# Optimization experiments

Measured on AMD Instinct MI355X. Metric: run time of the kernel, lower is better.

Reference implementation:

```python
import jax, jax.numpy as jnp
import numpy as np

NQ, NT, BSZ, E, NH = 100, 197, 128, 768, 12
HD = E // NH
EPS = 1e-12  # torch F.normalize default eps


def _l2norm(x, axis=-1):
    n = jnp.linalg.norm(x, axis=axis, keepdims=True)
    return x / jnp.maximum(n, EPS)


def setup_inputs() -> dict:
    rng = jax.random.key(0)
    ks = jax.random.split(rng, 10)
    s = 0.02  # xavier-ish scale for weights
    return {
        "query": jax.random.normal(ks[0], (NQ, BSZ, E), jnp.float32),
        "key": jax.random.normal(ks[1], (NT, BSZ, E), jnp.float32),
        "value": jax.random.normal(ks[2], (NT, BSZ, E), jnp.float32),
        "in_proj_weight": jax.random.normal(ks[3], (3 * E, E), jnp.float32) * s,
        "in_proj_bias": jnp.zeros((3 * E,), jnp.float32),
        "out_proj_weight": jax.random.normal(ks[4], (E, E), jnp.float32) * s,
        "out_proj_bias": jnp.zeros((E,), jnp.float32),
        "temperature": jnp.ones((NH, 1, 1), jnp.float32),
        "q_mapper": jax.random.normal(ks[5], (1, NT, NQ), jnp.float32),
        "x_mapper": jax.random.normal(ks[6], (1, NQ, NT), jnp.float32),
    }


def reference(query, key, value, in_proj_weight, in_proj_bias,
              out_proj_weight, out_proj_bias, temperature, q_mapper, x_mapper):
    nq, bsz, e = query.shape
    nt = key.shape[0]
    # packed in-projection: split into q/k/v weights
    wq, wk, wv = jnp.split(in_proj_weight, 3, axis=0)
    bq, bk, bv = jnp.split(in_proj_bias, 3, axis=0)
    q = query @ wq.T + bq   # [Nq, bsz, E]
    k = key @ wk.T + bk     # [Nt, bsz, E]
    v = value @ wv.T + bv   # [Nt, bsz, E]
    # reshape to [bsz, nh, hd, N] (channel-major for cross-covariance attn)
    q = q.reshape(nq, bsz, NH, HD).transpose(1, 2, 3, 0)  # [b, h, d, Nq]
    k = k.reshape(nt, bsz, NH, HD).transpose(1, 2, 3, 0)  # [b, h, d, Nt]
    v = v.reshape(nt, bsz, NH, HD).transpose(1, 2, 3, 0)  # [b, h, d, Nt]
    # normalize channel vectors over tokens
    qn = _l2norm(q)
    kn = _l2norm(k)
    # mappers: normalize over last dim, then shape to [Nq, Nt] operators
    qm_op = _l2norm(q_mapper[0])  # [Nt, Nq] normalized over Nq; transpose below
    xm_op = _l2norm(x_mapper[0])  # [Nq, Nt] normalized over Nt
    # qm = q @ q_mapper^T : [b,h,d,Nq] x [Nq,Nt] -> [b,h,d,Nt]
    qm = jnp.einsum('bhdq,tq->bhdt', qn, qm_op)
    # cross-covariance attention over channels: [b,h,d,d]
    attn = jnp.einsum('bhdt,bhet->bhde', qm, kn) * temperature[None]  # temp [nh,1,1] broadcasts per-head
    attn = jax.nn.softmax(attn, axis=-1)
    x = jnp.einsum('bhde,bhet->bhdt', attn, v)        # [b,h,d,Nt]
    out = jnp.einsum('bhdt,qt->bhdq', x, xm_op)       # [b,h,d,Nq]
    # back to [Nq, bsz, E]
    out = out.transpose(3, 0, 1, 2).reshape(nq, bsz, e)
    out = out @ out_proj_weight.T + out_proj_bias
    return out
```

## Files before the change

kernel.cpp:

```cpp
#include <hip/hip_runtime.h>
#include <hip/hip_bf16.h>

using bf16 = __hip_bfloat16;

constexpr int NQ  = 100;
constexpr int NT  = 197;
constexpr int BSZ = 128;
constexpr int EMB = 768;
constexpr int NHD = 12;
constexpr int HDD = 64;
constexpr int COLS = BSZ * EMB;
constexpr int M_Q  = NQ * BSZ;
constexpr int M_KV = NT * BSZ;
constexpr int TPAD = 224;

constexpr size_t SZ_Q16  = (size_t)M_Q  * EMB * 2;
constexpr size_t SZ_KV16 = (size_t)M_KV * EMB * 2;
constexpr size_t SZ_WI   = (size_t)3 * EMB * EMB * 2;
constexpr size_t SZ_T16  = (size_t)COLS * TPAD * 2;
constexpr size_t SZ_128  = (size_t)COLS * 128 * 2;
constexpr size_t OFF_QB   = 256;
constexpr size_t OFF_KB   = OFF_QB + SZ_Q16;
constexpr size_t OFF_VB   = OFF_KB + SZ_KV16;
constexpr size_t OFF_WI   = OFF_VB + SZ_KV16;
constexpr size_t OFF_QP16 = OFF_WI + SZ_WI;
constexpr size_t OFF_KP16 = OFF_QP16 + SZ_Q16;
constexpr size_t OFF_VP16 = OFF_KP16 + SZ_KV16;
constexpr size_t OFF_QMNT = OFF_VP16 + SZ_KV16;
constexpr size_t OFF_XMNT = OFF_QMNT + 57344;
constexpr size_t OFF_WO   = OFF_XMNT + 57344;
constexpr size_t OFF_KPT  = 256;
constexpr size_t OFF_VPT  = OFF_KPT + SZ_T16;
constexpr size_t OFF_W16T = OFF_VPT + SZ_T16;
constexpr size_t OFF_QNT  = OFF_KP16;
constexpr size_t OFF_G16  = OFF_VP16;
constexpr size_t OFF_XO   = 256;

__device__ __forceinline__ float dl(const float* p) { return *p; }
__device__ __forceinline__ float dl(const bf16* p) { return __bfloat162float(*p); }

__device__ __forceinline__ ushort f2bf(float x) {
    union { float f; unsigned u; } v; v.f = x;
    unsigned r = v.u + 0x7FFFu + ((v.u >> 16) & 1u);
    return (ushort)(r >> 16);
}
__device__ __forceinline__ float bf2f(ushort x) {
    union { unsigned u; float f; } v; v.u = (unsigned)x << 16;
    return v.f;
}
__device__ __forceinline__ void dstore(float* p, float v) { *p = v; }
__device__ __forceinline__ void dstore(bf16* p, float v) { *p = __float2bfloat16(v); }

typedef __attribute__((ext_vector_type(8))) short short8;
typedef __attribute__((ext_vector_type(4))) short shortv4;
typedef __attribute__((ext_vector_type(4))) float f32x4;

__device__ __forceinline__ void gload16(const bf16* g, ushort* l) {
    __builtin_amdgcn_global_load_lds(
        (const __attribute__((address_space(1))) unsigned int*)g,
        (__attribute__((address_space(3))) unsigned int*)l, 16, 0, 0);
}

__device__ __forceinline__ int2 xcd_swz(int bx, int by, int gx, int gy) {
    const int nwg = gx * gy;
    const int L = by * gx + bx;
    const int q = nwg >> 3, r = nwg & 7;
    const int c = L & 7, i = L >> 3;
    const int wg = (c < r ? c * (q + 1) : r * (q + 1) + (c - r) * q) + i;
    return make_int2(wg % gx, wg / gx);
}

__global__ void k_zero(float* p, int n) {
    int i = blockIdx.x * 256 + threadIdx.x;
    if (i < n) p[i] = 0.f;
}

__global__ __launch_bounds__(256) void k_cvt5(
        const float* __restrict__ s0, bf16* __restrict__ d0,
        const float* __restrict__ s1, bf16* __restrict__ d1,
        const float* __restrict__ s2, bf16* __restrict__ d2,
        const float* __restrict__ s3, bf16* __restrict__ d3,
        const float* __restrict__ s4, bf16* __restrict__ d4) {
    int bk = blockIdx.x;
    const float* s; bf16* d; int lb;
    if      (bk < 864)   { s = s0; d = d0; lb = bk; }
    else if (bk < 5664)  { s = s1; d = d1; lb = bk - 864; }
    else if (bk < 15120) { s = s2; d = d2; lb = bk - 5664; }
    else if (bk < 24576) { s = s3; d = d3; lb = bk - 15120; }
    else                 { s = s4; d = d4; lb = bk - 24576; }
    size_t i = ((size_t)lb * 256 + threadIdx.x) * 8;
    float4 a = *(const float4*)(s + i), b = *(const float4*)(s + i + 4);
    short8 r;
    r[0] = (short)f2bf(a.x); r[1] = (short)f2bf(a.y); r[2] = (short)f2bf(a.z); r[3] = (short)f2bf(a.w);
    r[4] = (short)f2bf(b.x); r[5] = (short)f2bf(b.y); r[6] = (short)f2bf(b.z); r[7] = (short)f2bf(b.w);
    *(short8*)(d + i) = r;
}

template <typename T>
__global__ __launch_bounds__(128) void k_qmn(const T* qm, bf16* dstT) {
    __shared__ float red[128];
    int t = blockIdx.x, q = threadIdx.x;
    float v = (q < NQ) ? dl(&qm[t * NQ + q]) : 0.f;
    red[q] = v * v;
    __syncthreads();
    for (int s = 64; s > 0; s >>= 1) { if (q < s) red[q] += red[q + s]; __syncthreads(); }
    float inv = 1.f / fmaxf(sqrtf(red[0]), 1e-12f);
    if (q < NQ) dstore(&dstT[(size_t)q * TPAD + t], v * inv);
}

template <typename T>
__global__ __launch_bounds__(256) void k_xmn(const T* xm, bf16* dstT) {
    __shared__ float red[256];
    int q = blockIdx.x, t = threadIdx.x;
    float v = (t < NT) ? dl(&xm[q * NT + t]) : 0.f;
    red[t] = v * v;
    __syncthreads();
    for (int s = 128; s > 0; s >>= 1) { if (t < s) red[t] += red[t + s]; __syncthreads(); }
    float inv = 1.f / fmaxf(sqrtf(red[0]), 1e-12f);
    if (t < NT) dstore(&dstT[(size_t)q * TPAD + t], v * inv);
}

template <int NR, int TP, int NORM>
__global__ __launch_bounds__(256) void k_trn(const bf16* __restrict__ src,
        bf16* __restrict__ dst) {
    __shared__ ushort tile[TP * 73];
    __shared__ float ssp[4][64];
    __shared__ float inv_s[64];
    const int col0 = blockIdx.x * 64;
    const int tid = threadIdx.x;
    const int c = tid & 63, tb = tid >> 6;
    float ss = 0.f;
#pragma unroll
    for (int it = 0; it < TP / 4; ++it) {
        int t = tb + it * 4;
        ushort v = 0;
        if (t < NR) v = *(const ushort*)&src[(size_t)t * COLS + col0 + c];
        tile[t * 73 + c] = v;
        if (NORM) { float f = bf2f(v); ss = fmaf(f, f, ss); }
    }
    if (NORM) {
        ssp[tb][c] = ss;
        __syncthreads();
        if (tid < 64) {
            float s = ssp[0][tid] + ssp[1][tid] + ssp[2][tid] + ssp[3][tid];
            inv_s[tid] = 1.f / fmaxf(sqrtf(s), 1e-12f);
        }
    }
    __syncthreads();
    constexpr int UPC = TP / 8;
#pragma unroll
    for (int it = 0; it < (64 * UPC) / 256; ++it) {
        int u = tid + it * 256;
        int cc = u / UPC, t0 = (u % UPC) * 8;
        float inv = NORM ? inv_s[cc] : 1.f;
        short8 s;
#pragma unroll
        for (int r = 0; r < 8; ++r) {
            ushort raw = tile[(t0 + r) * 73 + cc];
            s[r] = NORM ? (short)f2bf(bf2f(raw) * inv) : (short)raw;
        }
        *(short8*)&dst[(size_t)(col0 + cc) * TP + t0] = s;
    }
}

__global__ __launch_bounds__(256) void k_trn2(const bf16* __restrict__ kp,
        const bf16* __restrict__ vp, bf16* __restrict__ kpT, bf16* __restrict__ vpT) {
    __shared__ ushort tile[TPAD * 73];
    __shared__ float ssp[4][64];
    __shared__ float inv_s[64];
    const int bk = blockIdx.x;
    const bool vseg = bk >= 1536;
    const bf16* src = vseg ? vp : kp;
    bf16* dst = vseg ? vpT : kpT;
    const int col0 = (vseg ? bk - 1536 : bk) * 64;
    const int tid = threadIdx.x;
    const int c = tid & 63, tb = tid >> 6;
    float ss = 0.f;
#pragma unroll
    for (int it = 0; it < TPAD / 4; ++it) {
        int t = tb + it * 4;
        ushort v = 0;
        if (t < NT) v = *(const ushort*)&src[(size_t)t * COLS + col0 + c];
        tile[t * 73 + c] = v;
        if (!vseg) { float f = bf2f(v); ss = fmaf(f, f, ss); }
    }
    if (!vseg) {
        ssp[tb][c] = ss;
        __syncthreads();
        if (tid < 64) {
            float s = ssp[0][tid] + ssp[1][tid] + ssp[2][tid] + ssp[3][tid];
            inv_s[tid] = 1.f / fmaxf(sqrtf(s), 1e-12f);
        }
    }
    __syncthreads();
    constexpr int UPC = TPAD / 8;
#pragma unroll
    for (int it = 0; it < (64 * UPC) / 256; ++it) {
        int u = tid + it * 256;
        int cc = u / UPC, t0 = (u % UPC) * 8;
        float inv = vseg ? 1.f : inv_s[cc];
        short8 s;
#pragma unroll
        for (int r = 0; r < 8; ++r) {
            ushort raw = tile[(t0 + r) * 73 + cc];
            s[r] = vseg ? (short)raw : (short)f2bf(bf2f(raw) * inv);
        }
        *(short8*)&dst[(size_t)(col0 + cc) * TPAD + t0] = s;
    }
}

template <typename TBias>
__global__ __launch_bounds__(256) void k_proj(
        const bf16* __restrict__ Aq, const bf16* __restrict__ Ak, const bf16* __restrict__ Av,
        const bf16* __restrict__ Wi, bf16* __restrict__ Cq, bf16* __restrict__ Ck,
        bf16* __restrict__ Cv, const TBias* __restrict__ bias) {
    __shared__ __align__(16) ushort As[128 * 32];
    __shared__ __align__(16) ushort Bs[128 * 32];
    const int t = threadIdx.x;
    const int2 bxy = xcd_swz(blockIdx.x, blockIdx.y, gridDim.x, gridDim.y);
    int byy = bxy.y, seg, lby;
    if (byy < 100)      { seg = 0; lby = byy; }
    else if (byy < 297) { seg = 1; lby = byy - 100; }
    else                { seg = 2; lby = byy - 297; }
    const bf16* Ab = seg == 0 ? Aq : (seg == 1 ? Ak : Av);
    const bf16* Wb = Wi + (size_t)seg * EMB * EMB;
    bf16* C = seg == 0 ? Cq : (seg == 1 ? Ck : Cv);
    const TBias* bp = bias + seg * EMB;
    const int n0 = bxy.x * 128, m0 = lby * 128;
    const int ln = t & 63, wv = t >> 6;
    const int ln15 = ln & 15, q8 = ln >> 4;
    const int mw = (wv & 1) * 64, nw = (wv >> 1) * 64;

    const int sr = ln >> 2, sk = (ln & 3) * 8;
    const bf16* gA = Ab + (size_t)(m0 + wv * 32 + sr) * EMB + sk;
    const bf16* gB = Wb + (size_t)(n0 + wv * 32 + sr) * EMB + sk;
    const size_t r16 = (size_t)16 * EMB;
    ushort* lA = &As[wv * 1024];
    ushort* lB = &Bs[wv * 1024];

    f32x4 acc[4][4] = {};
    for (int k0 = 0; k0 < EMB; k0 += 32) {
        gload16(gA + k0,       lA);
        gload16(gA + r16 + k0, lA + 512);
        gload16(gB + k0,       lB);
        gload16(gB + r16 + k0, lB + 512);
        __syncthreads();
        short8 a[4], b[4];
#pragma unroll
        for (int i = 0; i < 4; ++i)
            a[i] = *(const short8*)&As[(mw + i * 16 + ln15) * 32 + q8 * 8];
#pragma unroll
        for (int j = 0; j < 4; ++j)
            b[j] = *(const short8*)&Bs[(nw + j * 16 + ln15) * 32 + q8 * 8];
#pragma unroll
        for (int i = 0; i < 4; ++i)
#pragma unroll
            for (int j = 0; j < 4; ++j)
                acc[i][j] = __builtin_amdgcn_mfma_f32_16x16x32_bf16(a[i], b[j], acc[i][j], 0, 0, 0);
        __syncthreads();
    }
#pragma unroll
    for (int j = 0; j < 4; ++j) {
        const int n = n0 + nw + j * 16 + ln15;
        const float bv = dl(&bp[n]);
#pragma unroll
        for (int i = 0; i < 4; ++i) {
            const int mb = m0 + mw + i * 16 + q8 * 4;
#pragma unroll
            for (int r = 0; r < 4; ++r)
                dstore(&C[(size_t)(mb + r) * EMB + n], acc[i][j][r] + bv);
        }
    }
}

__global__ __launch_bounds__(256) void k_gw(
        const bf16* __restrict__ kpT, const bf16* __restrict__ vpT,
        const bf16* __restrict__ qmnT, const bf16* __restrict__ xmnT,
        bf16* __restrict__ g16, bf16* __restrict__ w16T) {
    __shared__ __align__(16) ushort As[128 * 32];
    __shared__ __align__(16) ushort Bs[128 * 32];
    const int t = threadIdx.x;
    const int2 bxy = xcd_swz(blockIdx.x, blockIdx.y, gridDim.x, gridDim.y);
    const bool wseg = bxy.y >= 768;
    const int lby = wseg ? bxy.y - 768 : bxy.y;
    const bf16* Ab = wseg ? vpT : kpT;
    const bf16* Bb = wseg ? xmnT : qmnT;
    const int m0 = lby * 128;
    const int ln = t & 63, wv = t >> 6;
    const int ln15 = ln & 15, q8 = ln >> 4;
    const int mw = (wv & 1) * 64, nw = (wv >> 1) * 64;

    const int sr = ln >> 2, sk = (ln & 3) * 8;
    const bf16* gA = Ab + (size_t)(m0 + wv * 32 + sr) * TPAD + sk;
    const bf16* gB = Bb + (size_t)(wv * 32 + sr) * TPAD + sk;
    const size_t r16 = (size_t)16 * TPAD;
    ushort* lA = &As[wv * 1024];
    ushort* lB = &Bs[wv * 1024];

    f32x4 acc[4][4] = {};
    for (int k0 = 0; k0 < TPAD; k0 += 32) {
        gload16(gA + k0,       lA);
        gload16(gA + r16 + k0, lA + 512);
        gload16(gB + k0,       lB);
        gload16(gB + r16 + k0, lB + 512);
        __syncthreads();
        short8 a[4], b[4];
#pragma unroll
        for (int i = 0; i < 4; ++i)
            a[i] = *(const short8*)&As[(mw + i * 16 + ln15) * 32 + q8 * 8];
#pragma unroll
        for (int j = 0; j < 4; ++j)
            b[j] = *(const short8*)&Bs[(nw + j * 16 + ln15) * 32 + q8 * 8];
#pragma unroll
        for (int i = 0; i < 4; ++i)
#pragma unroll
            for (int j = 0; j < 4; ++j)
                acc[i][j] = __builtin_amdgcn_mfma_f32_16x16x32_bf16(a[i], b[j], acc[i][j], 0, 0, 0);
        __syncthreads();
    }
#pragma unroll
    for (int j = 0; j < 4; ++j) {
        const int n = nw + j * 16 + ln15;
#pragma unroll
        for (int i = 0; i < 4; ++i) {
            const int mb = m0 + mw + i * 16 + q8 * 4;
            if (wseg) {
                shortv4 s;
#pragma unroll
                for (int r = 0; r < 4; ++r) s[r] = (short)f2bf(acc[i][j][r]);
                *(shortv4*)&w16T[(size_t)n * COLS + mb] = s;
            } else {
#pragma unroll
                for (int r = 0; r < 4; ++r)
                    dstore(&g16[(size_t)(mb + r) * 128 + n], acc[i][j][r]);
            }
        }
    }
}

template <typename TC, typename TBias>
__global__ __launch_bounds__(256) void k_gemm_mfma(
        const bf16* __restrict__ Ab, const bf16* __restrict__ Wb,
        TC* __restrict__ C, const TBias* __restrict__ bias,
        int M, int N, int K, int ldc) {
    __shared__ __align__(16) ushort As[128 * 32];
    __shared__ __align__(16) ushort Bs[128 * 32];
    const int t = threadIdx.x;
    const int2 bxy = xcd_swz(blockIdx.x, blockIdx.y, gridDim.x, gridDim.y);
    const int n0 = bxy.x * 128, m0 = bxy.y * 128;
    const int ln = t & 63, wv = t >> 6;
    const int ln15 = ln & 15, q8 = ln >> 4;
    const int mw = (wv & 1) * 64, nw = (wv >> 1) * 64;

    const int sr = ln >> 2, sk = (ln & 3) * 8;
    const bf16* gA = Ab + (size_t)(m0 + wv * 32 + sr) * K + sk;
    const bf16* gB = Wb + (size_t)(n0 + wv * 32 + sr) * K + sk;
    const size_t r16 = (size_t)16 * K;
    ushort* lA = &As[wv * 1024];
    ushort* lB = &Bs[wv * 1024];

    f32x4 acc[4][4] = {};
    for (int k0 = 0; k0 < K; k0 += 32) {
        gload16(gA + k0,       lA);
        gload16(gA + r16 + k0, lA + 512);
        gload16(gB + k0,       lB);
        gload16(gB + r16 + k0, lB + 512);
        __syncthreads();
        short8 a[4], b[4];
#pragma unroll
        for (int i = 0; i < 4; ++i)
            a[i] = *(const short8*)&As[(mw + i * 16 + ln15) * 32 + q8 * 8];
#pragma unroll
        for (int j = 0; j < 4; ++j)
            b[j] = *(const short8*)&Bs[(nw + j * 16 + ln15) * 32 + q8 * 8];
#pragma unroll
        for (int i = 0; i < 4; ++i)
#pragma unroll
            for (int j = 0; j < 4; ++j)
                acc[i][j] = __builtin_amdgcn_mfma_f32_16x16x32_bf16(a[i], b[j], acc[i][j], 0, 0, 0);
        __syncthreads();
    }
#pragma unroll
    for (int j = 0; j < 4; ++j) {
        const int n = n0 + nw + j * 16 + ln15;
        const float bv = dl(&bias[n]);
#pragma unroll
        for (int i = 0; i < 4; ++i) {
            const int mb = m0 + mw + i * 16 + q8 * 4;
#pragma unroll
            for (int r = 0; r < 4; ++r)
                dstore(&C[(size_t)(mb + r) * ldc + n], acc[i][j][r] + bv);
        }
    }
}

template <typename T>
__global__ __launch_bounds__(256) void k_attn(
        const bf16* __restrict__ qnT, const bf16* __restrict__ g16,
        const bf16* __restrict__ w16T, const T* __restrict__ temp,
        bf16* __restrict__ xo) {
    const int h = blockIdx.x, b = blockIdx.y;
    const int tid = threadIdx.x;
    const int ln = tid & 63, wv = tid >> 6;
    const int ln15 = ln & 15, q8 = ln >> 4;
    const int colbase = b * EMB + h * HDD;
    __shared__ __align__(16) ushort smem[16384];
    char* sm = (char*)smem;

#pragma unroll
    for (int it = 0; it < 4; ++it) {
        int u = tid + it * 256;
        int e = u >> 4, q0 = (u & 15) * 8;
        short8 s = *(const short8*)&g16[(size_t)(colbase + e) * 128 + q0];
        *(short8*)(sm + ((e * 256 + q0 * 2) ^ ((e & 7) << 4))) = s;
    }
#pragma unroll
    for (int it = 0; it < 4; ++it) {
        int u = tid + it * 256;
        int d = u >> 4, q0 = (u & 15) * 8;
        short8 s = *(const short8*)&qnT[(size_t)(colbase + d) * 128 + q0];
        *(short8*)(sm + 16384 + ((d * 256 + q0 * 2) ^ ((d & 7) << 4))) = s;
    }
    __syncthreads();

    const int drow = 16 * wv + ln15;
    f32x4 acc[4] = {};
#pragma unroll
    for (int ks = 0; ks < 4; ++ks) {
        short8 bfrag = *(const short8*)(sm + 16384 +
            ((drow * 256 + ks * 64 + q8 * 16) ^ ((drow & 7) << 4)));
#pragma unroll
        for (int i = 0; i < 4; ++i) {
            int erow = i * 16 + ln15;
            short8 afrag = *(const short8*)(sm +
                ((erow * 256 + ks * 64 + q8 * 16) ^ ((erow & 7) << 4)));
            acc[i] = __builtin_amdgcn_mfma_f32_16x16x32_bf16(afrag, bfrag, acc[i], 0, 0, 0);
        }
    }

    const float tv = dl(&temp[h]);
    float p[4][4];
    float mx = -1e30f;
#pragma unroll
    for (int i = 0; i < 4; ++i)
#pragma unroll
        for (int r = 0; r < 4; ++r) { p[i][r] = acc[i][r] * tv; mx = fmaxf(mx, p[i][r]); }
    mx = fmaxf(mx, __shfl_xor(mx, 16, 64));
    mx = fmaxf(mx, __shfl_xor(mx, 32, 64));
    float sum = 0.f;
#pragma unroll
    for (int i = 0; i < 4; ++i)
#pragma unroll
        for (int r = 0; r < 4; ++r) { p[i][r] = __expf(p[i][r] - mx); sum += p[i][r]; }
    sum += __shfl_xor(sum, 16, 64);
    sum += __shfl_xor(sum, 32, 64);
    const float rs = 1.f / sum;

    __syncthreads();

#pragma unroll
    for (int i = 0; i < 4; ++i) {
        shortv4 s4;
#pragma unroll
        for (int r = 0; r < 4; ++r) s4[r] = (short)f2bf(p[i][r] * rs);
        *(shortv4*)(sm + 16384 + drow * 144 + q8 * 8 + 32 * i) = s4;
    }
#pragma unroll
    for (int it = 0; it < 4; ++it) {
        int u = tid + it * 256;
        int q = u >> 3, e0 = (u & 7) * 8;
        short8 s = *(const short8*)&w16T[(size_t)q * COLS + colbase + e0];
        *(short8*)(sm + ((q * 128 + e0 * 2) ^ ((q & 7) << 4))) = s;
    }
    __syncthreads();

    f32x4 o[7] = {};
#pragma unroll
    for (int ks = 0; ks < 2; ++ks) {
        short8 afrag = *(const short8*)(sm + 16384 + drow * 144 + ks * 64 + q8 * 16);
#pragma unroll
        for (int j = 0; j < 7; ++j) {
            int qrow = j * 16 + ln15;
            short8 bfrag = *(const short8*)(sm +
                ((qrow * 128 + ks * 64 + q8 * 16) ^ ((qrow & 7) << 4)));
            o[j] = __builtin_amdgcn_mfma_f32_16x16x32_bf16(afrag, bfrag, o[j], 0, 0, 0);
        }
    }
    const int dbase = h * HDD + 16 * wv + q8 * 4;
#pragma unroll
    for (int j = 0; j < 7; ++j) {
        int q = j * 16 + ln15;
        if (q < NQ) {
            shortv4 s4;
#pragma unroll
            for (int r = 0; r < 4; ++r) s4[r] = (short)f2bf(o[j][r]);
            *(shortv4*)&xo[(size_t)(q * BSZ + b) * EMB + dbase] = s4;
        }
    }
}

extern "C" void kernel_launch(void* const* d_in, const int* in_sizes, int n_in,
                              void* d_out, int out_size, void* d_ws, size_t ws_size,
                              hipStream_t stream) {
    char* ws = (char*)d_ws;
    bf16* qb16  = (bf16*)(ws + OFF_QB);
    bf16* kb16  = (bf16*)(ws + OFF_KB);
    bf16* vb16  = (bf16*)(ws + OFF_VB);
    bf16* wi16  = (bf16*)(ws + OFF_WI);
    bf16* qp16  = (bf16*)(ws + OFF_QP16);
    bf16* kp16  = (bf16*)(ws + OFF_KP16);
    bf16* vp16  = (bf16*)(ws + OFF_VP16);
    bf16* qmnT  = (bf16*)(ws + OFF_QMNT);
    bf16* xmnT  = (bf16*)(ws + OFF_XMNT);
    bf16* wo16  = (bf16*)(ws + OFF_WO);
    bf16* kpT   = (bf16*)(ws + OFF_KPT);
    bf16* vpT   = (bf16*)(ws + OFF_VPT);
    bf16* w16T  = (bf16*)(ws + OFF_W16T);
    bf16* qnT   = (bf16*)(ws + OFF_QNT);
    bf16* g16   = (bf16*)(ws + OFF_G16);
    bf16* xo16  = (bf16*)(ws + OFF_XO);

    const bool isbf = (in_sizes[0] == 19660800);

    k_zero<<<112, 256, 0, stream>>>((float*)(ws + OFF_QMNT), 28672);

    if (isbf) {
        k_qmn<bf16><<<197, 128, 0, stream>>>((const bf16*)d_in[8], qmnT);
        k_xmn<bf16><<<100, 256, 0, stream>>>((const bf16*)d_in[9], xmnT);
        k_proj<bf16><<<dim3(6, 494), 256, 0, stream>>>(
            (const bf16*)d_in[0], (const bf16*)d_in[1], (const bf16*)d_in[2],
            (const bf16*)d_in[3], qp16, kp16, vp16, (const bf16*)d_in[4]);
        k_trn2<<<3072, 256, 0, stream>>>(kp16, vp16, kpT, vpT);
        k_trn<NQ, 128, 1><<<COLS / 64, 256, 0, stream>>>(qp16, qnT);
        k_gw<<<dim3(1, 1536), 256, 0, stream>>>(kpT, vpT, qmnT, xmnT, g16, w16T);
        k_attn<bf16><<<dim3(NHD, BSZ), 256, 0, stream>>>(
            qnT, g16, w16T, (const bf16*)d_in[7], xo16);
        k_gemm_mfma<bf16, bf16><<<dim3(6, 100), 256, 0, stream>>>(
            xo16, (const bf16*)d_in[5], (bf16*)d_out, (const bf16*)d_in[6],
            M_Q, EMB, EMB, EMB);
    } else {
        k_qmn<float><<<197, 128, 0, stream>>>((const float*)d_in[8], qmnT);
        k_xmn<float><<<100, 256, 0, stream>>>((const float*)d_in[9], xmnT);
        k_cvt5<<<24864, 256, 0, stream>>>(
            (const float*)d_in[3], wi16,
            (const float*)d_in[0], qb16,
            (const float*)d_in[1], kb16,
            (const float*)d_in[2], vb16,
            (const float*)d_in[5], wo16);
        k_proj<float><<<dim3(6, 494), 256, 0, stream>>>(
            qb16, kb16, vb16, wi16, qp16, kp16, vp16, (const float*)d_in[4]);
        k_trn2<<<3072, 256, 0, stream>>>(kp16, vp16, kpT, vpT);
        k_trn<NQ, 128, 1><<<COLS / 64, 256, 0, stream>>>(qp16, qnT);
        k_gw<<<dim3(1, 1536), 256, 0, stream>>>(kpT, vpT, qmnT, xmnT, g16, w16T);
        k_attn<float><<<dim3(NHD, BSZ), 256, 0, stream>>>(
            qnT, g16, w16T, (const float*)d_in[7], xo16);
        k_gemm_mfma<float, float><<<dim3(6, 100), 256, 0, stream>>>(
            xo16, wo16, (float*)d_out, (const float*)d_in[6], M_Q, EMB, EMB, EMB);
    }
}
```

Before: 477.3 us.

## Replace QKV projection GEMM with 256x256 double-buffered pipelined MFMA kernel

Adds k_mm8, a 512-thread kernel for the fused Q/K/V in-projection on the float-input path. It computes 256x256 output tiles with a 64-wide K step. The kernel double-buffers LDS and issues the next stage's global-to-LDS loads between MFMA quads, using explicit waitcnt, barriers and setprio. The aim is more data reuse per tile and overlap of memory traffic with matrix math, compared with the 128x128 single-buffered kernel it replaces. K/V workspace buffers are padded to a multiple of 256 rows so the last tiles can read and write out of range safely. The 128 KB of LDS per block limits occupancy to roughly one block per CU, and the bf16-input path is left on the old kernel.

```diff
diff --git a/kernel.cpp b/kernel.cpp
--- a/kernel.cpp
+++ b/kernel.cpp
@@ -10,23 +10,24 @@
 constexpr int NHD = 12;
 constexpr int HDD = 64;
 constexpr int COLS = BSZ * EMB;
-constexpr int M_Q  = NQ * BSZ;
-constexpr int M_KV = NT * BSZ;
+constexpr int M_Q  = 12800;
+constexpr int M_KV = 25216;
+constexpr int M_KVP = 25344;
 constexpr int TPAD = 224;
 
 constexpr size_t SZ_Q16  = (size_t)M_Q  * EMB * 2;
 constexpr size_t SZ_KV16 = (size_t)M_KV * EMB * 2;
+constexpr size_t SZ_KVP  = (size_t)M_KVP * EMB * 2;
 constexpr size_t SZ_WI   = (size_t)3 * EMB * EMB * 2;
 constexpr size_t SZ_T16  = (size_t)COLS * TPAD * 2;
-constexpr size_t SZ_128  = (size_t)COLS * 128 * 2;
 constexpr size_t OFF_QB   = 256;
 constexpr size_t OFF_KB   = OFF_QB + SZ_Q16;
 constexpr size_t OFF_VB   = OFF_KB + SZ_KV16;
 constexpr size_t OFF_WI   = OFF_VB + SZ_KV16;
 constexpr size_t OFF_QP16 = OFF_WI + SZ_WI;
 constexpr size_t OFF_KP16 = OFF_QP16 + SZ_Q16;
-constexpr size_t OFF_VP16 = OFF_KP16 + SZ_KV16;
-constexpr size_t OFF_QMNT = OFF_VP16 + SZ_KV16;
+constexpr size_t OFF_VP16 = OFF_KP16 + SZ_KVP;
+constexpr size_t OFF_QMNT = OFF_VP16 + SZ_KVP;
 constexpr size_t OFF_XMNT = OFF_QMNT + 57344;
 constexpr size_t OFF_WO   = OFF_XMNT + 57344;
 constexpr size_t OFF_KPT  = 256;
@@ -209,8 +210,95 @@
     }
 }
 
+#define MM8_BAR  { __builtin_amdgcn_s_barrier(); __builtin_amdgcn_sched_barrier(0); }
+#define MM8_LGK0 { asm volatile("s_waitcnt lgkmcnt(0)" ::: "memory"); __builtin_amdgcn_sched_barrier(0); }
+#define MM8_VM8  { asm volatile("s_waitcnt vmcnt(8)" ::: "memory"); __builtin_amdgcn_sched_barrier(0); }
+#define MM8_VM0  { asm volatile("s_waitcnt vmcnt(0)" ::: "memory"); __builtin_amdgcn_sched_barrier(0); }
+#define MM8_STAGE(CUR, ISB, H, KT) do { \
+    const bf16* gb_ = (ISB) ? (Wb + (size_t)(n0 + (H)*128 + srow) * EMB + (KT)*64 + skcol) \
+                            : (Ab + (size_t)(m0 + (H)*128 + srow) * EMB + (KT)*64 + skcol); \
+    ushort* lb_ = ((ISB) ? B_lds : A_lds) + (CUR)*16384 + (H)*8192 + wid*512; \
+    gload16(gb_, lb_); \
+    gload16(gb_ + (size_t)64 * EMB, lb_ + 4096); \
+} while (0)
+#define MM8_LOADFRAGS(CUR, KK, AARR, BARR) { \
+    _Pragma("unroll") for (int m_ = 0; m_ < 8; ++m_) \
+        AARR[m_] = *(const short8*)&A_lds[(CUR)*16384 + (wr*128 + m_*16 + ln15)*64 + (KK)*32 + q8*8]; \
+    _Pragma("unroll") for (int j_ = 0; j_ < 4; ++j_) \
+        BARR[j_] = *(const short8*)&B_lds[(CUR)*16384 + (wc*64 + j_*16 + ln15)*64 + (KK)*32 + q8*8]; }
+#define MM8_QUAD(AARR, BARR, MB) { \
+    __builtin_amdgcn_s_setprio(1); \
+    _Pragma("unroll") for (int m_ = 0; m_ < 4; ++m_) \
+        _Pragma("unroll") for (int j_ = 0; j_ < 4; ++j_) \
+            acc[(MB) + m_][j_] = __builtin_amdgcn_mfma_f32_16x16x32_bf16( \
+                AARR[(MB) + m_], BARR[j_], acc[(MB) + m_][j_], 0, 0, 0); \
+    __builtin_amdgcn_s_setprio(0); }
+
+__global__ __launch_bounds__(512, 2) void k_mm8(
+        const bf16* __restrict__ A0, const bf16* __restrict__ A1, const bf16* __restrict__ A2,
+        const bf16* __restrict__ W,
+        bf16* __restrict__ C0, bf16* __restrict__ C1, bf16* __restrict__ C2,
+        const float* __restrict__ bias, int mt0, int mt01) {
+    __shared__ __align__(16) ushort A_lds[2 * 16384];
+    __shared__ __align__(16) ushort B_lds[2 * 16384];
+    const int tid = threadIdx.x;
+    const int2 bxy = xcd_swz(blockIdx.x, blockIdx.y, gridDim.x, gridDim.y);
+    int seg = 0, lby = bxy.y;
+    if (bxy.y < mt0)       { seg = 0; lby = bxy.y; }
+    else if (bxy.y < mt01) { seg = 1; lby = bxy.y - mt0; }
+    else                   { seg = 2; lby = bxy.y - mt01; }
+    const bf16* Ab = seg == 0 ? A0 : (seg == 1 ? A1 : A2);
+    const bf16* Wb = W + (size_t)seg * EMB * EMB;
+    bf16* C = seg == 0 ? C0 : (seg == 1 ? C1 : C2);
+    const float* bp = bias + seg * EMB;
+    const int m0 = lby * 256, n0 = bxy.x * 256;
+    const int wid = tid >> 6, ln = tid & 63;
+    const int wr = wid >> 2, wc = wid & 3;
+    const int ln15 = ln & 15, q8 = ln >> 4;
+    const int srow = tid >> 3, skcol = (tid & 7) * 8;
+
+    f32x4 acc[8][4] = {};
+    short8 a0[8], b0[4], a1[8], b1[4];
+
+    MM8_STAGE(0, 0, 0, 0); MM8_STAGE(0, 0, 1, 0); MM8_STAGE(0, 1, 0, 0); MM8_STAGE(0, 1, 1, 0);
+    MM8_STAGE(1, 0, 0, 1); MM8_STAGE(1, 0, 1, 1); MM8_STAGE(1, 1, 0, 1); MM8_STAGE(1, 1, 1, 1);
+    MM8_VM8;
+    MM8_BAR;
+
+    for (int t = 0; t < 12; ++t) {
+        const int c = t & 1, nxt = t + 2;
+        MM8_LOADFRAGS(c, 0, a0, b0);
+        MM8_QUAD(a0, b0, 0);
+        MM8_BAR;
+        MM8_LOADFRAGS(c, 1, a1, b1);
+        MM8_QUAD(a0, b0, 4);
+        MM8_LGK0;
+        MM8_BAR;
+        if (nxt < 12) { MM8_STAGE(c, 0, 0, nxt); MM8_STAGE(c, 0, 1, nxt); }
+        MM8_QUAD(a1, b1, 0);
+        MM8_BAR;
+        if (nxt < 12) { MM8_STAGE(c, 1, 0, nxt); MM8_STAGE(c, 1, 1, nxt); }
+        if (t < 10) { MM8_VM8; } else { MM8_VM0; }
+        MM8_QUAD(a1, b1, 4);
+        MM8_BAR;
+    }
+
+#pragma unroll
+    for (int j = 0; j < 4; ++j) {
+        const int n = n0 + wc * 64 + j * 16 + ln15;
+        const float bv = bp[n];
+#pragma unroll
+        for (int m = 0; m < 8; ++m) {
+            const int mb = m0 + wr * 128 + m * 16 + q8 * 4;
+#pragma unroll
+            for (int r = 0; r < 4; ++r)
+                dstore(&C[(size_t)(mb + r) * EMB + n], acc[m][j][r] + bv);
+        }
+    }
+}
+
 template <typename TBias>
-__global__ __launch_bounds__(256) void k_proj(
+__global__ __launch_bounds__(256) void k_proj2(
         const bf16* __restrict__ Aq, const bf16* __restrict__ Ak, const bf16* __restrict__ Av,
         const bf16* __restrict__ Wi, bf16* __restrict__ Cq, bf16* __restrict__ Ck,
         bf16* __restrict__ Cv, const TBias* __restrict__ bias) {
@@ -230,14 +318,12 @@
     const int ln = t & 63, wv = t >> 6;
     const int ln15 = ln & 15, q8 = ln >> 4;
     const int mw = (wv & 1) * 64, nw = (wv >> 1) * 64;
-
     const int sr = ln >> 2, sk = (ln & 3) * 8;
     const bf16* gA = Ab + (size_t)(m0 + wv * 32 + sr) * EMB + sk;
     const bf16* gB = Wb + (size_t)(n0 + wv * 32 + sr) * EMB + sk;
     const size_t r16 = (size_t)16 * EMB;
     ushort* lA = &As[wv * 1024];
     ushort* lB = &Bs[wv * 1024];
-
     f32x4 acc[4][4] = {};
     for (int k0 = 0; k0 < EMB; k0 += 32) {
         gload16(gA + k0,       lA);
@@ -289,14 +375,12 @@
     const int ln = t & 63, wv = t >> 6;
     const int ln15 = ln & 15, q8 = ln >> 4;
     const int mw = (wv & 1) * 64, nw = (wv >> 1) * 64;
-
     const int sr = ln >> 2, sk = (ln & 3) * 8;
     const bf16* gA = Ab + (size_t)(m0 + wv * 32 + sr) * TPAD + sk;
     const bf16* gB = Bb + (size_t)(wv * 32 + sr) * TPAD + sk;
     const size_t r16 = (size_t)16 * TPAD;
     ushort* lA = &As[wv * 1024];
     ushort* lB = &Bs[wv * 1024];
-
     f32x4 acc[4][4] = {};
     for (int k0 = 0; k0 < TPAD; k0 += 32) {
         gload16(gA + k0,       lA);
@@ -351,14 +435,12 @@
     const int ln = t & 63, wv = t >> 6;
     const int ln15 = ln & 15, q8 = ln >> 4;
     const int mw = (wv & 1) * 64, nw = (wv >> 1) * 64;
-
     const int sr = ln >> 2, sk = (ln & 3) * 8;
     const bf16* gA = Ab + (size_t)(m0 + wv * 32 + sr) * K + sk;
     const bf16* gB = Wb + (size_t)(n0 + wv * 32 + sr) * K + sk;
     const size_t r16 = (size_t)16 * K;
     ushort* lA = &As[wv * 1024];
     ushort* lB = &Bs[wv * 1024];
-
     f32x4 acc[4][4] = {};
     for (int k0 = 0; k0 < K; k0 += 32) {
         gload16(gA + k0,       lA);
@@ -527,7 +609,7 @@
     if (isbf) {
         k_qmn<bf16><<<197, 128, 0, stream>>>((const bf16*)d_in[8], qmnT);
         k_xmn<bf16><<<100, 256, 0, stream>>>((const bf16*)d_in[9], xmnT);
-        k_proj<bf16><<<dim3(6, 494), 256, 0, stream>>>(
+        k_proj2<bf16><<<dim3(6, 494), 256, 0, stream>>>(
             (const bf16*)d_in[0], (const bf16*)d_in[1], (const bf16*)d_in[2],
             (const bf16*)d_in[3], qp16, kp16, vp16, (const bf16*)d_in[4]);
         k_trn2<<<3072, 256, 0, stream>>>(kp16, vp16, kpT, vpT);
@@ -547,8 +629,9 @@
             (const float*)d_in[1], kb16,
             (const float*)d_in[2], vb16,
             (const float*)d_in[5], wo16);
-        k_proj<float><<<dim3(6, 494), 256, 0, stream>>>(
-            qb16, kb16, vb16, wi16, qp16, kp16, vp16, (const float*)d_in[4]);
+        k_mm8<<<dim3(3, 248), 512, 0, stream>>>(
+            qb16, kb16, vb16, wi16, qp16, kp16, vp16,
+            (const float*)d_in[4], 50, 149);
         k_trn2<<<3072, 256, 0, stream>>>(kp16, vp16, kpT, vpT);
         k_trn<NQ, 128, 1><<<COLS / 64, 256, 0, stream>>>(qp16, qnT);
         k_gw<<<dim3(1, 1536), 256, 0, stream>>>(kpT, vpT, qmnT, xmnT, g16, w16T);
```

After: 491.5 us. +3.0%, slower.
